# Kernel optimization log

Hardware: AMD Instinct MI355X
Metric: run time of the kernel (lower is better)

Reference implementation:

```python
import jax, jax.numpy as jnp
import numpy as np

HIDDEN = 1024
HEADS = 16
HEAD_DIM = HIDDEN // HEADS  # 64
ROPE_DIM = 64
ROPE_BASE = 10000.0
B, T = 2, 2048


def setup_inputs() -> dict:
    key = jax.random.key(0)
    k1, k2, k3, k4, k5, k6 = jax.random.split(key, 6)
    x = jax.random.normal(k1, (B, T, HIDDEN), dtype=jnp.float32)
    input_ids = jax.random.randint(k2, (B, T), 0, 32000)
    # torch Linear weights: [out_features, in_features]
    qkv_w = jax.random.normal(k3, (3 * HIDDEN, HIDDEN), dtype=jnp.float32) * (1.0 / np.sqrt(HIDDEN))
    qkv_b = jnp.zeros((3 * HIDDEN,), dtype=jnp.float32)
    out_w = jax.random.normal(k4, (HIDDEN, HIDDEN), dtype=jnp.float32) * (1.0 / np.sqrt(HIDDEN))
    out_b = jnp.zeros((HIDDEN,), dtype=jnp.float32)
    global_idx = jnp.array([0, 1, 2], dtype=jnp.int64)  # special_tokens values
    return {"x": x, "input_ids": input_ids, "qkv_w": qkv_w, "qkv_b": qkv_b,
            "out_w": out_w, "out_b": out_b, "global_idx": global_idx}


def _rope_cos_sin(t, offset=0):
    inv_freq = 1.0 / (ROPE_BASE ** (jnp.arange(0, ROPE_DIM, 2, dtype=jnp.float32) / ROPE_DIM))  # [ROPE_DIM/2]
    pos = jnp.arange(offset, offset + t, dtype=jnp.float32)
    freqs = pos[:, None] * inv_freq[None, :]  # [T, ROPE_DIM/2]
    return jnp.cos(freqs)[None, None], jnp.sin(freqs)[None, None]  # [1,1,T,ROPE_DIM/2]


def _apply_rotary(x, cos, sin):
    x_rot, x_pass = x[..., :ROPE_DIM], x[..., ROPE_DIM:]
    half = ROPE_DIM // 2
    x1, x2 = x_rot[..., :half], x_rot[..., half:]
    return jnp.concatenate([x1 * cos - x2 * sin, x1 * sin + x2 * cos, x_pass], axis=-1)


def reference(x, input_ids, qkv_w, qkv_b, out_w, out_b, global_idx):
    b, t, _ = x.shape
    qkv = x @ qkv_w.T + qkv_b  # [B,T,3*HIDDEN]
    q, k, v = jnp.split(qkv, 3, axis=-1)
    # -> [B, H, T, Dh]
    reshape = lambda z: z.reshape(b, t, HEADS, HEAD_DIM).transpose(0, 2, 1, 3)
    q, k, v = reshape(q), reshape(k), reshape(v)
    cos, sin = _rope_cos_sin(t)
    q = _apply_rotary(q, cos, sin)
    k = _apply_rotary(k, cos, sin)
    # causal + global-query mask
    causal = jnp.tril(jnp.ones((t, t), dtype=bool))[None, None]  # [1,1,T,T]
    global_mask = jnp.isin(input_ids, global_idx)  # [B,T]
    allow = causal | global_mask[:, None, :, None]  # [B,1,T,T]
    scale = jnp.sqrt(jnp.float32(HEAD_DIM))
    logits = jnp.einsum('bhqd,bhkd->bhqk', q, k) / scale
    neg = -jnp.finfo(logits.dtype).max
    logits = jnp.where(allow, logits, neg)
    attn = jax.nn.softmax(logits, axis=-1)
    out = jnp.einsum('bhqk,bhkd->bhqd', attn, v)  # [B,H,T,Dh]
    out = out.transpose(0, 2, 1, 3).reshape(b, t, HEADS * HEAD_DIM)
    return out @ out_w.T + out_b
```

## Files before the change

kernel.cpp:

```cpp
#include <hip/hip_runtime.h>
#include <hip/hip_bf16.h>
#include <math.h>

typedef __bf16 bf16;
typedef __bf16 bf16x8 __attribute__((ext_vector_type(8)));
typedef float floatx4 __attribute__((ext_vector_type(4)));

#define HIDDEN 1024
#define NHEADS 16
#define HDIM 64
#define TSEQ 2048
#define NBATCH 2
#define MTOT (NBATCH * TSEQ)

__device__ inline void glds16(bf16* lds, const bf16* g)
{
  __builtin_amdgcn_global_load_lds(
      (const __attribute__((address_space(1))) unsigned int*)g,
      (__attribute__((address_space(3))) unsigned int*)lds, 16, 0, 0);
}

__global__ __launch_bounds__(256) void cvt_f32_bf16(
    const float* __restrict__ src, bf16* __restrict__ dst, int n)
{
  const int i = (blockIdx.x * 256 + threadIdx.x) * 8;
  if (i >= n) return;
  const floatx4 u = *(const floatx4*)(src + i);
  const floatx4 v = *(const floatx4*)(src + i + 4);
  bf16x8 r;
#pragma unroll
  for (int j = 0; j < 4; j++) { r[j] = (bf16)u[j]; r[4 + j] = (bf16)v[j]; }
  *(bf16x8*)(dst + i) = r;
}

template <int MODE>
__global__ __launch_bounds__(256) void gemm_bt(
    const bf16* __restrict__ A, const bf16* __restrict__ W,
    const float* __restrict__ bias, float* __restrict__ C,
    bf16* __restrict__ Qb, bf16* __restrict__ Kb, bf16* __restrict__ Vb,
    int M, int N, int K)
{
  __shared__ bf16 As[128 * 32];
  __shared__ bf16 Bs[128 * 32];

  const int tid  = threadIdx.x;
  const int lane = tid & 63;
  const int wv   = tid >> 6;
  const int quad = lane >> 4;
  const int l16  = lane & 15;
  const int m0 = blockIdx.y * 128;
  const int n0 = blockIdx.x * 128;
  const int wm = (wv >> 1) * 64;
  const int wn = (wv & 1) * 64;

  const int srow = lane >> 2;
  const int scol = (lane & 3) * 8;

  floatx4 acc[4][4];
#pragma unroll
  for (int i = 0; i < 4; i++)
#pragma unroll
    for (int j = 0; j < 4; j++) acc[i][j] = (floatx4){0.f, 0.f, 0.f, 0.f};

  for (int k0 = 0; k0 < K; k0 += 32) {
    __syncthreads();
    const bf16* ga = A + (size_t)(m0 + wv * 32 + srow) * K + k0 + scol;
    glds16(As + (wv * 32) * 32, ga);
    glds16(As + (wv * 32 + 16) * 32, ga + (size_t)16 * K);
    const bf16* gb = W + (size_t)(n0 + wv * 32 + srow) * K + k0 + scol;
    glds16(Bs + (wv * 32) * 32, gb);
    glds16(Bs + (wv * 32 + 16) * 32, gb + (size_t)16 * K);
    __syncthreads();

    bf16x8 af[4], bfr[4];
#pragma unroll
    for (int i = 0; i < 4; i++)
      af[i] = *(const bf16x8*)(As + (wm + i * 16 + l16) * 32 + quad * 8);
#pragma unroll
    for (int j = 0; j < 4; j++)
      bfr[j] = *(const bf16x8*)(Bs + (wn + j * 16 + l16) * 32 + quad * 8);
#pragma unroll
    for (int i = 0; i < 4; i++)
#pragma unroll
      for (int j = 0; j < 4; j++)
        acc[i][j] = __builtin_amdgcn_mfma_f32_16x16x32_bf16(af[i], bfr[j], acc[i][j], 0, 0, 0);
  }

#pragma unroll
  for (int i = 0; i < 4; i++) {
    const int gmBase = m0 + wm + i * 16 + quad * 4;
#pragma unroll
    for (int j = 0; j < 4; j++) {
      const int gn = n0 + wn + j * 16 + l16;
      const float bs = bias[gn];
#pragma unroll
      for (int r = 0; r < 4; r++) {
        const int gm = gmBase + r;
        const float v = acc[i][j][r] + bs;
        if (MODE == 1) {
          C[(size_t)gm * N + gn] = v;
        } else {
          const int which = gn >> 10;
          const int rem = gn & 1023;
          const int h = rem >> 6, d = rem & 63;
          const int b = gm >> 11, t = gm & 2047;
          bf16* dst = (which == 0) ? Qb : (which == 1) ? Kb : Vb;
          dst[((size_t)(b * NHEADS + h) * TSEQ + t) * HDIM + d] = (bf16)v;
        }
      }
    }
  }
}

__global__ __launch_bounds__(256) void rope_kernel(bf16* __restrict__ Q,
                                                   bf16* __restrict__ K)
{
  const int idx = blockIdx.x * 256 + threadIdx.x;
  if (idx >= 32 * TSEQ * 32) return;
  const int i  = idx & 31;
  const int t  = (idx >> 5) & (TSEQ - 1);
  const int bh = idx >> 16;
  const float inv = powf(10000.0f, -(float)i * (1.0f / 32.0f));
  const float ang = (float)t * inv;
  float s, c;
  sincosf(ang, &s, &c);
  const size_t base = ((size_t)bh * TSEQ + t) * HDIM;
  {
    const float x1 = (float)Q[base + i], x2 = (float)Q[base + i + 32];
    Q[base + i]      = (bf16)(x1 * c - x2 * s);
    Q[base + i + 32] = (bf16)(x1 * s + x2 * c);
  }
  {
    const float x1 = (float)K[base + i], x2 = (float)K[base + i + 32];
    K[base + i]      = (bf16)(x1 * c - x2 * s);
    K[base + i + 32] = (bf16)(x1 * s + x2 * c);
  }
}

__global__ __launch_bounds__(256) void transpose_v(const bf16* __restrict__ V,
                                                   bf16* __restrict__ Vt)
{
  __shared__ bf16 tile[64][80];
  const int bh = blockIdx.y;
  const int t0 = blockIdx.x * 64;
  const bf16* src = V + ((size_t)bh * TSEQ + t0) * HDIM;
  for (int c = threadIdx.x; c < 512; c += 256) {
    const int r = c >> 3, c8 = (c & 7) * 8;
    *(bf16x8*)&tile[r][c8] = *(const bf16x8*)(src + (size_t)r * HDIM + c8);
  }
  __syncthreads();
  bf16* dst = Vt + (size_t)bh * HDIM * TSEQ + t0;
  for (int c = threadIdx.x; c < 512; c += 256) {
    const int d = c >> 3, t8 = (c & 7) * 8;
    bf16x8 vv;
#pragma unroll
    for (int j = 0; j < 8; j++) vv[j] = tile[t8 + j][d];
    *(bf16x8*)(dst + (size_t)d * TSEQ + t8) = vv;
  }
}

__device__ inline int swz(int g) { return (g & ~7) | ((g ^ (g >> 3) ^ (g >> 6)) & 7); }

__global__ __launch_bounds__(256) void attn_kernel(
    const bf16* __restrict__ Q, const bf16* __restrict__ K,
    const bf16* __restrict__ Vt, bf16* __restrict__ O,
    const int* __restrict__ ids, const int* __restrict__ gidx)
{
  __shared__ bf16 Ks[4096];
  __shared__ bf16 Vs[4096];
  __shared__ int flags[4];

  const int tid  = threadIdx.x;
  const int lane = tid & 63;
  const int wv   = tid >> 6;
  const int quad = lane >> 4;
  const int l16  = lane & 15;
  const int bh = blockIdx.y;
  const int b  = bh >> 4;
  const int h  = bh & 15;

  const bf16* Qp = Q + (size_t)bh * TSEQ * HDIM;
  const bf16* Kp = K + (size_t)bh * TSEQ * HDIM;
  const bf16* Vp = Vt + (size_t)bh * HDIM * TSEQ;

  const int rK  = tid >> 3;
  const int dcK = tid & 7;
  const int gk = ((rK >> 2) & 1) * 128 + (dcK >> 2) * 64 +
                 ((dcK & 3) * 16 + (((rK >> 3) << 2) | (rK & 3)));
  const int kd0 = swz(gk) * 8, kd1 = swz(gk + 256) * 8;
  const int dV = tid >> 3;
  const int uV = tid & 7;
  const int gv = (uV >> 2) * 256 + (dV >> 4) * 64 + ((uV & 3) * 16 + (dV & 15));
  const int vd0 = swz(gv) * 8, vd1 = swz(gv + 128) * 8;

  const int g0v = gidx[0], g1v = gidx[1], g2v = gidx[2];

#pragma unroll
  for (int ph = 0; ph < 2; ph++) {
    const int qt = ph ? (31 - (int)blockIdx.x) : (int)blockIdx.x;
    const int q0 = qt * 64 + wv * 16;

    const bf16x8 qf0 = *(const bf16x8*)(Qp + (size_t)(q0 + l16) * HDIM + quad * 8);
    const bf16x8 qf1 = *(const bf16x8*)(Qp + (size_t)(q0 + l16) * HDIM + 32 + quad * 8);

    const int myq = q0 + l16;
    const int myid = ids[b * TSEQ + myq];
    const int gl = (myid == g0v) | (myid == g1v) | (myid == g2v);
    flags[wv] = __any(gl);
    __syncthreads();
    const int anyg = flags[0] | flags[1] | flags[2] | flags[3];
    const int kmax = anyg ? TSEQ : (qt * 64 + 64);

    float lsum = 0.f;
    floatx4 o[4];
#pragma unroll
    for (int nt = 0; nt < 4; nt++) o[nt] = (floatx4){0.f, 0.f, 0.f, 0.f};

    bf16x8 kA = *(const bf16x8*)(Kp + tid * 8);
    bf16x8 kB = *(const bf16x8*)(Kp + 2048 + tid * 8);
    bf16x8 vA = *(const bf16x8*)(Vp + (size_t)dV * TSEQ + uV * 8);
    bf16x8 vB = *(const bf16x8*)(Vp + (size_t)(dV + 32) * TSEQ + uV * 8);

    for (int k0 = 0; k0 < kmax; k0 += 64) {
      __syncthreads();
      *(bf16x8*)(Ks + kd0) = kA;
      *(bf16x8*)(Ks + kd1) = kB;
      *(bf16x8*)(Vs + vd0) = vA;
      *(bf16x8*)(Vs + vd1) = vB;
      __syncthreads();

      if (k0 + 64 < kmax) {
        const bf16* kc = Kp + (size_t)(k0 + 64) * HDIM;
        kA = *(const bf16x8*)(kc + tid * 8);
        kB = *(const bf16x8*)(kc + 2048 + tid * 8);
        vA = *(const bf16x8*)(Vp + (size_t)dV * TSEQ + k0 + 64 + uV * 8);
        vB = *(const bf16x8*)(Vp + (size_t)(dV + 32) * TSEQ + k0 + 64 + uV * 8);
      }

#pragma unroll
      for (int g = 0; g < 2; g++) {
        const int kb = k0 + g * 32;
        const int rb = g * 256 + lane;
        const bf16x8 a00 = *(const bf16x8*)(Ks + swz(rb) * 8);
        const bf16x8 a01 = *(const bf16x8*)(Ks + swz(rb + 64) * 8);
        const bf16x8 a10 = *(const bf16x8*)(Ks + swz(rb + 128) * 8);
        const bf16x8 a11 = *(const bf16x8*)(Ks + swz(rb + 192) * 8);
        floatx4 s0 = (floatx4){0.f, 0.f, 0.f, 0.f};
        floatx4 s1 = (floatx4){0.f, 0.f, 0.f, 0.f};
        s0 = __builtin_amdgcn_mfma_f32_16x16x32_bf16(a00, qf0, s0, 0, 0, 0);
        s0 = __builtin_amdgcn_mfma_f32_16x16x32_bf16(a01, qf1, s0, 0, 0, 0);
        s1 = __builtin_amdgcn_mfma_f32_16x16x32_bf16(a10, qf0, s1, 0, 0, 0);
        s1 = __builtin_amdgcn_mfma_f32_16x16x32_bf16(a11, qf1, s1, 0, 0, 0);

        bf16x8 pf;
#pragma unroll
        for (int r = 0; r < 4; r++) {
          const int key0 = kb + quad * 8 + r;
          const int key1 = key0 + 4;
          const float p0 = (gl || key0 <= myq) ? __expf(s0[r] * 0.125f) : 0.f;
          const float p1 = (gl || key1 <= myq) ? __expf(s1[r] * 0.125f) : 0.f;
          lsum += p0 + p1;
          pf[r]     = (bf16)p0;
          pf[4 + r] = (bf16)p1;
        }

#pragma unroll
        for (int nt = 0; nt < 4; nt++) {
          const bf16x8 vf = *(const bf16x8*)(Vs + swz(g * 256 + nt * 64 + lane) * 8);
          o[nt] = __builtin_amdgcn_mfma_f32_16x16x32_bf16(pf, vf, o[nt], 0, 0, 0);
        }
      }
    }

    lsum += __shfl_xor(lsum, 16);
    lsum += __shfl_xor(lsum, 32);

#pragma unroll
    for (int r = 0; r < 4; r++) {
      const float inv = 1.0f / __shfl(lsum, quad * 4 + r);
      const int q = q0 + quad * 4 + r;
      const size_t rowoff = ((size_t)b * TSEQ + q) * HIDDEN + h * HDIM;
#pragma unroll
      for (int nt = 0; nt < 4; nt++)
        O[rowoff + nt * 16 + l16] = (bf16)(o[nt][r] * inv);
    }
  }
}

extern "C" void kernel_launch(void* const* d_in, const int* in_sizes, int n_in,
                              void* d_out, int out_size, void* d_ws, size_t ws_size,
                              hipStream_t stream)
{
  const float* x     = (const float*)d_in[0];
  const int*   ids   = (const int*)d_in[1];
  const float* qkv_w = (const float*)d_in[2];
  const float* qkv_b = (const float*)d_in[3];
  const float* out_w = (const float*)d_in[4];
  const float* out_b = (const float*)d_in[5];
  const int*   gidx  = (const int*)d_in[6];
  float* out = (float*)d_out;

  char* ws = (char*)d_ws;
  bf16* Q      = (bf16*)(ws);
  bf16* Kb     = (bf16*)(ws + (size_t)(8u << 20));
  bf16* V      = (bf16*)(ws + (size_t)(16u << 20));
  bf16* slot24 = (bf16*)(ws + (size_t)(24u << 20));
  bf16* xb     = slot24;
  bf16* Vt     = slot24;
  bf16* out_wb = slot24;
  bf16* qkv_wb = (bf16*)d_out;
  bf16* O      = V;

  cvt_f32_bf16<<<2048, 256, 0, stream>>>(x, xb, MTOT * HIDDEN);
  cvt_f32_bf16<<<1536, 256, 0, stream>>>(qkv_w, qkv_wb, 3 * HIDDEN * HIDDEN);
  gemm_bt<0><<<dim3(3072 / 128, MTOT / 128), 256, 0, stream>>>(
      xb, qkv_wb, qkv_b, nullptr, Q, Kb, V, MTOT, 3 * HIDDEN, HIDDEN);
  rope_kernel<<<(32 * TSEQ * 32) / 256, 256, 0, stream>>>(Q, Kb);
  transpose_v<<<dim3(TSEQ / 64, 32), 256, 0, stream>>>(V, Vt);
  attn_kernel<<<dim3(16, 32), 256, 0, stream>>>(Q, Kb, Vt, O, ids, gidx);
  cvt_f32_bf16<<<512, 256, 0, stream>>>(out_w, out_wb, HIDDEN * HIDDEN);
  gemm_bt<1><<<dim3(HIDDEN / 128, MTOT / 128), 256, 0, stream>>>(
      O, out_wb, out_b, out, nullptr, nullptr, nullptr, MTOT, HIDDEN, HIDDEN);
}
```

Measured before the change: 214.9 us.

## Merge prep and mid kernels, shrink GEMM N-tile, convert out_w inline, remap attention blocks

Merges the x and qkv_w conversions into one launch, and merges the RoPE and V-transpose kernels into one launch, to cut launch overhead. The GEMM N-tile drops from 128 to 64 to roughly double the number of blocks, and the output projection now reads fp32 out_w and converts it to bf16 while staging into LDS, so the separate weight-conversion kernel goes away. The attention grid is flattened to 1D, with heads grouped per XCD and the order of the two query tiles each block handles swapped, aiming for better L2 locality and load balance. In exchange, the narrower GEMM tiles load A more times and do fewer MFMAs per LDS load, and the fp32 weight path adds per-k-step global loads and conversions.

```diff
diff --git a/kernel.cpp b/kernel.cpp
--- a/kernel.cpp
+++ b/kernel.cpp
@@ -20,11 +20,14 @@
       (__attribute__((address_space(3))) unsigned int*)lds, 16, 0, 0);
 }
 
-__global__ __launch_bounds__(256) void cvt_f32_bf16(
-    const float* __restrict__ src, bf16* __restrict__ dst, int n)
-{
-  const int i = (blockIdx.x * 256 + threadIdx.x) * 8;
-  if (i >= n) return;
+__global__ __launch_bounds__(256) void prep_kernel(
+    const float* __restrict__ x, bf16* __restrict__ xb,
+    const float* __restrict__ qkv_w, bf16* __restrict__ qkv_wb)
+{
+  const int bid = blockIdx.x;
+  const float* src = (bid < 2048) ? x : qkv_w;
+  bf16* dst = (bid < 2048) ? xb : qkv_wb;
+  const int i = (((bid < 2048) ? bid : bid - 2048) * 256 + threadIdx.x) * 8;
   const floatx4 u = *(const floatx4*)(src + i);
   const floatx4 v = *(const floatx4*)(src + i + 4);
   bf16x8 r;
@@ -33,15 +36,15 @@
   *(bf16x8*)(dst + i) = r;
 }
 
-template <int MODE>
+template <int MODE, bool WF32>
 __global__ __launch_bounds__(256) void gemm_bt(
-    const bf16* __restrict__ A, const bf16* __restrict__ W,
+    const bf16* __restrict__ A, const void* __restrict__ Wv,
     const float* __restrict__ bias, float* __restrict__ C,
     bf16* __restrict__ Qb, bf16* __restrict__ Kb, bf16* __restrict__ Vb,
     int M, int N, int K)
 {
   __shared__ bf16 As[128 * 32];
-  __shared__ bf16 Bs[128 * 32];
+  __shared__ bf16 Bs[64 * 32];
 
   const int tid  = threadIdx.x;
   const int lane = tid & 63;
@@ -49,40 +52,55 @@
   const int quad = lane >> 4;
   const int l16  = lane & 15;
   const int m0 = blockIdx.y * 128;
-  const int n0 = blockIdx.x * 128;
-  const int wm = (wv >> 1) * 64;
-  const int wn = (wv & 1) * 64;
+  const int n0 = blockIdx.x * 64;
+  const int wm = (wv & 1) * 64;
+  const int wn = (wv >> 1) * 32;
 
   const int srow = lane >> 2;
   const int scol = (lane & 3) * 8;
-
-  floatx4 acc[4][4];
+  const int rW = tid >> 2;
+  const int cW = (tid & 3) * 8;
+
+  floatx4 acc[4][2];
 #pragma unroll
   for (int i = 0; i < 4; i++)
 #pragma unroll
-    for (int j = 0; j < 4; j++) acc[i][j] = (floatx4){0.f, 0.f, 0.f, 0.f};
+    for (int j = 0; j < 2; j++) acc[i][j] = (floatx4){0.f, 0.f, 0.f, 0.f};
 
   for (int k0 = 0; k0 < K; k0 += 32) {
+    floatx4 wf0, wf1;
+    if (WF32) {
+      const float* wp = (const float*)Wv + (size_t)(n0 + rW) * K + k0 + cW;
+      wf0 = *(const floatx4*)wp;
+      wf1 = *(const floatx4*)(wp + 4);
+    }
     __syncthreads();
+    if (WF32) {
+      bf16x8 wb;
+#pragma unroll
+      for (int j = 0; j < 4; j++) { wb[j] = (bf16)wf0[j]; wb[4 + j] = (bf16)wf1[j]; }
+      *(bf16x8*)(Bs + rW * 32 + cW) = wb;
+    }
     const bf16* ga = A + (size_t)(m0 + wv * 32 + srow) * K + k0 + scol;
     glds16(As + (wv * 32) * 32, ga);
     glds16(As + (wv * 32 + 16) * 32, ga + (size_t)16 * K);
-    const bf16* gb = W + (size_t)(n0 + wv * 32 + srow) * K + k0 + scol;
-    glds16(Bs + (wv * 32) * 32, gb);
-    glds16(Bs + (wv * 32 + 16) * 32, gb + (size_t)16 * K);
+    if (!WF32) {
+      const bf16* gb = (const bf16*)Wv + (size_t)(n0 + wv * 16 + srow) * K + k0 + scol;
+      glds16(Bs + (wv * 16) * 32, gb);
+    }
     __syncthreads();
 
-    bf16x8 af[4], bfr[4];
+    bf16x8 af[4], bfr[2];
 #pragma unroll
     for (int i = 0; i < 4; i++)
       af[i] = *(const bf16x8*)(As + (wm + i * 16 + l16) * 32 + quad * 8);
 #pragma unroll
-    for (int j = 0; j < 4; j++)
+    for (int j = 0; j < 2; j++)
       bfr[j] = *(const bf16x8*)(Bs + (wn + j * 16 + l16) * 32 + quad * 8);
 #pragma unroll
     for (int i = 0; i < 4; i++)
 #pragma unroll
-      for (int j = 0; j < 4; j++)
+      for (int j = 0; j < 2; j++)
         acc[i][j] = __builtin_amdgcn_mfma_f32_16x16x32_bf16(af[i], bfr[j], acc[i][j], 0, 0, 0);
   }
 
@@ -90,72 +108,72 @@
   for (int i = 0; i < 4; i++) {
     const int gmBase = m0 + wm + i * 16 + quad * 4;
 #pragma unroll
-    for (int j = 0; j < 4; j++) {
+    for (int j = 0; j < 2; j++) {
       const int gn = n0 + wn + j * 16 + l16;
       const float bs = bias[gn];
-#pragma unroll
-      for (int r = 0; r < 4; r++) {
-        const int gm = gmBase + r;
-        const float v = acc[i][j][r] + bs;
-        if (MODE == 1) {
-          C[(size_t)gm * N + gn] = v;
-        } else {
-          const int which = gn >> 10;
-          const int rem = gn & 1023;
-          const int h = rem >> 6, d = rem & 63;
-          const int b = gm >> 11, t = gm & 2047;
-          bf16* dst = (which == 0) ? Qb : (which == 1) ? Kb : Vb;
-          dst[((size_t)(b * NHEADS + h) * TSEQ + t) * HDIM + d] = (bf16)v;
+      if (MODE == 1) {
+#pragma unroll
+        for (int r = 0; r < 4; r++)
+          C[(size_t)(gmBase + r) * N + gn] = acc[i][j][r] + bs;
+      } else {
+        const int which = gn >> 10;
+        const int rem = gn & 1023;
+        const int h = rem >> 6, d = rem & 63;
+        bf16* dst = (which == 0) ? Qb : (which == 1) ? Kb : Vb;
+#pragma unroll
+        for (int r = 0; r < 4; r++) {
+          const int gm = gmBase + r;
+          const int b_ = gm >> 11, t = gm & 2047;
+          dst[((size_t)(b_ * NHEADS + h) * TSEQ + t) * HDIM + d] =
+              (bf16)(acc[i][j][r] + bs);
         }
       }
     }
   }
 }
 
-__global__ __launch_bounds__(256) void rope_kernel(bf16* __restrict__ Q,
-                                                   bf16* __restrict__ K)
-{
-  const int idx = blockIdx.x * 256 + threadIdx.x;
-  if (idx >= 32 * TSEQ * 32) return;
-  const int i  = idx & 31;
-  const int t  = (idx >> 5) & (TSEQ - 1);
-  const int bh = idx >> 16;
-  const float inv = powf(10000.0f, -(float)i * (1.0f / 32.0f));
-  const float ang = (float)t * inv;
-  float s, c;
-  sincosf(ang, &s, &c);
-  const size_t base = ((size_t)bh * TSEQ + t) * HDIM;
-  {
-    const float x1 = (float)Q[base + i], x2 = (float)Q[base + i + 32];
-    Q[base + i]      = (bf16)(x1 * c - x2 * s);
-    Q[base + i + 32] = (bf16)(x1 * s + x2 * c);
-  }
-  {
-    const float x1 = (float)K[base + i], x2 = (float)K[base + i + 32];
-    K[base + i]      = (bf16)(x1 * c - x2 * s);
-    K[base + i + 32] = (bf16)(x1 * s + x2 * c);
-  }
-}
-
-__global__ __launch_bounds__(256) void transpose_v(const bf16* __restrict__ V,
-                                                   bf16* __restrict__ Vt)
+__global__ __launch_bounds__(256) void mid_kernel(
+    bf16* __restrict__ Q, bf16* __restrict__ K,
+    const bf16* __restrict__ V, bf16* __restrict__ Vt)
 {
   __shared__ bf16 tile[64][80];
-  const int bh = blockIdx.y;
-  const int t0 = blockIdx.x * 64;
-  const bf16* src = V + ((size_t)bh * TSEQ + t0) * HDIM;
-  for (int c = threadIdx.x; c < 512; c += 256) {
-    const int r = c >> 3, c8 = (c & 7) * 8;
-    *(bf16x8*)&tile[r][c8] = *(const bf16x8*)(src + (size_t)r * HDIM + c8);
-  }
-  __syncthreads();
-  bf16* dst = Vt + (size_t)bh * HDIM * TSEQ + t0;
-  for (int c = threadIdx.x; c < 512; c += 256) {
-    const int d = c >> 3, t8 = (c & 7) * 8;
-    bf16x8 vv;
-#pragma unroll
-    for (int j = 0; j < 8; j++) vv[j] = tile[t8 + j][d];
-    *(bf16x8*)(dst + (size_t)d * TSEQ + t8) = vv;
+  if (blockIdx.x < 8192) {
+    const int idx = blockIdx.x * 256 + threadIdx.x;
+    const int i  = idx & 31;
+    const int t  = (idx >> 5) & (TSEQ - 1);
+    const int bh = idx >> 16;
+    const float inv = powf(10000.0f, -(float)i * (1.0f / 32.0f));
+    float s, c;
+    sincosf((float)t * inv, &s, &c);
+    const size_t base = ((size_t)bh * TSEQ + t) * HDIM;
+    {
+      const float x1 = (float)Q[base + i], x2 = (float)Q[base + i + 32];
+      Q[base + i]      = (bf16)(x1 * c - x2 * s);
+      Q[base + i + 32] = (bf16)(x1 * s + x2 * c);
+    }
+    {
+      const float x1 = (float)K[base + i], x2 = (float)K[base + i + 32];
+      K[base + i]      = (bf16)(x1 * c - x2 * s);
+      K[base + i + 32] = (bf16)(x1 * s + x2 * c);
+    }
+  } else {
+    const int bid = blockIdx.x - 8192;
+    const int bh = bid >> 5;
+    const int t0 = (bid & 31) * 64;
+    const bf16* src = V + ((size_t)bh * TSEQ + t0) * HDIM;
+    for (int c = threadIdx.x; c < 512; c += 256) {
+      const int r = c >> 3, c8 = (c & 7) * 8;
+      *(bf16x8*)&tile[r][c8] = *(const bf16x8*)(src + (size_t)r * HDIM + c8);
+    }
+    __syncthreads();
+    bf16* dst = Vt + (size_t)bh * HDIM * TSEQ + t0;
+    for (int c = threadIdx.x; c < 512; c += 256) {
+      const int d = c >> 3, t8 = (c & 7) * 8;
+      bf16x8 vv;
+#pragma unroll
+      for (int j = 0; j < 8; j++) vv[j] = tile[t8 + j][d];
+      *(bf16x8*)(dst + (size_t)d * TSEQ + t8) = vv;
+    }
   }
 }
 
@@ -175,7 +193,11 @@
   const int wv   = tid >> 6;
   const int quad = lane >> 4;
   const int l16  = lane & 15;
-  const int bh = blockIdx.y;
+
+  const int xcd = blockIdx.x & 7;
+  const int j   = blockIdx.x >> 3;
+  const int bh  = xcd * 4 + (j >> 4);
+  const int p   = j & 15;
   const int b  = bh >> 4;
   const int h  = bh & 15;
 
@@ -197,7 +219,7 @@
 
 #pragma unroll
   for (int ph = 0; ph < 2; ph++) {
-    const int qt = ph ? (31 - (int)blockIdx.x) : (int)blockIdx.x;
+    const int qt = ph ? p : (31 - p);
     const int q0 = qt * 64 + wv * 16;
 
     const bf16x8 qf0 = *(const bf16x8*)(Qp + (size_t)(q0 + l16) * HDIM + quad * 8);
@@ -307,18 +329,14 @@
   bf16* slot24 = (bf16*)(ws + (size_t)(24u << 20));
   bf16* xb     = slot24;
   bf16* Vt     = slot24;
-  bf16* out_wb = slot24;
   bf16* qkv_wb = (bf16*)d_out;
   bf16* O      = V;
 
-  cvt_f32_bf16<<<2048, 256, 0, stream>>>(x, xb, MTOT * HIDDEN);
-  cvt_f32_bf16<<<1536, 256, 0, stream>>>(qkv_w, qkv_wb, 3 * HIDDEN * HIDDEN);
-  gemm_bt<0><<<dim3(3072 / 128, MTOT / 128), 256, 0, stream>>>(
+  prep_kernel<<<3584, 256, 0, stream>>>(x, xb, qkv_w, qkv_wb);
+  gemm_bt<0, false><<<dim3(3072 / 64, MTOT / 128), 256, 0, stream>>>(
       xb, qkv_wb, qkv_b, nullptr, Q, Kb, V, MTOT, 3 * HIDDEN, HIDDEN);
-  rope_kernel<<<(32 * TSEQ * 32) / 256, 256, 0, stream>>>(Q, Kb);
-  transpose_v<<<dim3(TSEQ / 64, 32), 256, 0, stream>>>(V, Vt);
-  attn_kernel<<<dim3(16, 32), 256, 0, stream>>>(Q, Kb, Vt, O, ids, gidx);
-  cvt_f32_bf16<<<512, 256, 0, stream>>>(out_w, out_wb, HIDDEN * HIDDEN);
-  gemm_bt<1><<<dim3(HIDDEN / 128, MTOT / 128), 256, 0, stream>>>(
-      O, out_wb, out_b, out, nullptr, nullptr, nullptr, MTOT, HIDDEN, HIDDEN);
-}
+  mid_kernel<<<9216, 256, 0, stream>>>(Q, Kb, V, Vt);
+  attn_kernel<<<512, 256, 0, stream>>>(Q, Kb, Vt, O, ids, gidx);
+  gemm_bt<1, true><<<dim3(HIDDEN / 64, MTOT / 128), 256, 0, stream>>>(
+      O, out_w, out_b, out, nullptr, nullptr, nullptr, MTOT, HIDDEN, HIDDEN);
+}
```

Result: slower. 223.7 us (+4.1%).
